# Kernel tuning notes

Measured on AMD Instinct MI355X. Metric: run time of the kernel, lower is better.

## Reference

```python
import jax, jax.numpy as jnp
import numpy as np
import math

B, L, DM, DI, DS, DR, K, NL = 1, 1024, 768, 1536, 16, 48, 4, 2
DT_MIN, DT_MAX = 0.001, 0.1


def rmsnorm(x, w, eps=1e-5):
    return x * jax.lax.rsqrt(jnp.mean(x * x, axis=-1, keepdims=True) + eps) * w


def causal_dwconv(x, w, b):
    # x: [B,L,C], w: [C,1,K]. torch Conv1d(padding=K-1)[..., :L] == left-pad K-1 causal conv.
    y = jax.lax.conv_general_dilated(
        x.transpose(0, 2, 1), w, (1,), [(K - 1, 0)],
        dimension_numbers=('NCH', 'OIH', 'NCH'), feature_group_count=DI)
    return y.transpose(0, 2, 1) + b


def selective_scan(x, delta, A, Bm, Cm, D):
    # x, delta: [B,L,DI]; A: [DI,DS]; Bm, Cm: [B,L,DS]; D: [DI]
    dA = jnp.exp(delta[..., None] * A)               # [B,L,DI,DS]
    BX = (delta * x)[..., None] * Bm[:, :, None, :]  # [B,L,DI,DS]

    def comb(c1, c2):
        a1, b1 = c1
        a2, b2 = c2
        return (a1 * a2, a2 * b1 + b2)

    _, hs = jax.lax.associative_scan(comb, (dA, BX), axis=1)  # h_t = dA_t*h_{t-1} + BX_t
    return jnp.einsum('bldn,bln->bld', hs, Cm) + D * x


def ssm(x, xproj_w, dt_w, dt_b, A_log, D):
    dbc = jnp.einsum('bld,ed->ble', x, xproj_w)            # [B,L,DR+2*DS]
    dlt, Bm, Cm = jnp.split(dbc, [DR, DR + DS], axis=-1)
    delta = jax.nn.softplus(jnp.einsum('blr,dr->bld', dlt, dt_w) + dt_b)
    return selective_scan(x, delta, -jnp.exp(A_log), Bm, Cm, D)


def mamba_block(x, p):
    xz = jnp.einsum('bld,ed->ble', x, p['in_w'])           # [B,L,2*DI]
    xin, z = jnp.split(xz, 2, axis=-1)
    xf = jax.nn.silu(causal_dwconv(xin, p['cf_w'], p['cf_b']))
    xb = jax.nn.silu(causal_dwconv(xin[:, ::-1, :], p['cb_w'], p['cb_b']))
    yf = ssm(xf, p['xf_w'], p['dtf_w'], p['dtf_b'], p['Af'], p['Df'])
    yb = ssm(xb, p['xb_w'], p['dtb_w'], p['dtb_b'], p['Ab'], p['Db'])  # NOT flipped back (faithful)
    y = jnp.einsum('ble,de->bld', jnp.concatenate([yf, yb], axis=-1), p['pro_w']) + p['pro_b']
    # tokenizer: scores over L, softmax along L, mix values; dropout = identity (eval)
    att = jax.nn.softmax(jnp.einsum('bld,td->btl', y, p['wA']), axis=-1)  # [B,T=L,L]
    vv = jnp.einsum('bld,de->ble', y, p['wV'])
    y = jnp.einsum('btl,ble->bte', att, vv)
    return jnp.einsum('bld,od->blo', y * jax.nn.silu(z), p['out_w'])


def reference(x, norm_w, in_proj_w, conv_f_w, conv_f_b, conv_b_w, conv_b_b,
              xproj_f_w, xproj_b_w, dt_f_w, dt_f_b, dt_b_w, dt_b_b,
              A_log_f, D_f, A_log_b, D_b, out_w, token_wA, token_wV, pro_w, pro_b):
    for i in range(NL):
        p = dict(in_w=in_proj_w[i], cf_w=conv_f_w[i], cf_b=conv_f_b[i],
                 cb_w=conv_b_w[i], cb_b=conv_b_b[i], xf_w=xproj_f_w[i],
                 xb_w=xproj_b_w[i], dtf_w=dt_f_w[i], dtf_b=dt_f_b[i],
                 dtb_w=dt_b_w[i], dtb_b=dt_b_b[i], Af=A_log_f[i], Df=D_f[i],
                 Ab=A_log_b[i], Db=D_b[i], out_w=out_w[i], wA=token_wA[i],
                 wV=token_wV[i], pro_w=pro_w[i], pro_b=pro_b[i])
        x = x + mamba_block(rmsnorm(x, norm_w[i]), p)
    return x


def setup_inputs():
    key = jax.random.key(0)
    ks = jax.random.split(key, 16)
    rn = lambda k, sh, s=0.02: jax.random.normal(k, sh, jnp.float32) * s
    A_log = jnp.broadcast_to(jnp.log(jnp.arange(1, DS + 1, dtype=jnp.float32)), (NL, DI, DS))
    dt = jnp.exp(jax.random.uniform(ks[0], (NL, DI)) * (math.log(DT_MAX) - math.log(DT_MIN)) + math.log(DT_MIN))
    inv_dt = dt + jnp.log(-jnp.expm1(-dt))  # softplus^-1(dt)
    dt_std = DR ** -0.5
    kaiming = (2.0 / DI) ** 0.5
    return {
        'x': jax.random.normal(ks[1], (B, L, DM), jnp.float32),
        'norm_w': jnp.ones((NL, DM), jnp.float32),
        'in_proj_w': rn(ks[2], (NL, 2 * DI, DM)),
        'conv_f_w': rn(ks[3], (NL, DI, 1, K), 0.3),
        'conv_f_b': jnp.zeros((NL, DI), jnp.float32),
        'conv_b_w': rn(ks[4], (NL, DI, 1, K), 0.3),
        'conv_b_b': jnp.zeros((NL, DI), jnp.float32),
        'xproj_f_w': rn(ks[5], (NL, DR + 2 * DS, DI)),
        'xproj_b_w': rn(ks[6], (NL, DR + 2 * DS, DI)),
        'dt_f_w': jax.random.uniform(ks[7], (NL, DI, DR), jnp.float32, -dt_std, dt_std),
        'dt_f_b': inv_dt,
        'dt_b_w': jax.random.uniform(ks[8], (NL, DI, DR), jnp.float32, -dt_std, dt_std),
        'dt_b_b': inv_dt,
        'A_log_f': A_log,
        'D_f': jnp.ones((NL, DI), jnp.float32),
        'A_log_b': A_log,
        'D_b': jnp.ones((NL, DI), jnp.float32),
        'out_w': rn(ks[9], (NL, DM, DI)),
        'token_wA': rn(ks[10], (NL, L, DI), kaiming),
        'token_wV': rn(ks[11], (NL, DI, DI), kaiming),
        'pro_w': rn(ks[12], (NL, DI, 2 * DI)),
        'pro_b': jnp.zeros((NL, DI), jnp.float32),
    }
```

## Files before the change

### kernel.cpp

```cpp
#include <hip/hip_runtime.h>
#include <hip/hip_bf16.h>
#include <math.h>
#include <stdint.h>

#define LSEQ 1024
#define DMODEL 768
#define DINNER 1536
#define DSTATE 16
#define DRANK 48
#define KCONV 4
#define NLAYER 2
#define DBC 80
#define NQ 8
#define QL (LSEQ / NQ)
#define SCH 8
#define SCW 32
#define QCH (QL / SCH)

typedef unsigned short u16;
typedef __attribute__((ext_vector_type(8))) __bf16 bf16x8;
typedef __attribute__((ext_vector_type(4))) float f32x4;
typedef __attribute__((ext_vector_type(4))) unsigned short us4;

__device__ __forceinline__ u16 f2bf(float f) {
  union { float f; unsigned u; } v; v.f = f;
  unsigned r = v.u + 0x7fffu + ((v.u >> 16) & 1u);
  return (u16)(r >> 16);
}
__device__ __forceinline__ float bf2f(u16 u) {
  union { unsigned u; float f; } v; v.u = ((unsigned)u) << 16;
  return v.f;
}

__device__ __forceinline__ void gload16(const void* g, void* l) {
  auto gp = reinterpret_cast<const __attribute__((address_space(1))) uint32_t*>(
      reinterpret_cast<uintptr_t>(g));
  auto lp = reinterpret_cast<__attribute__((address_space(3))) uint32_t*>(
      reinterpret_cast<uintptr_t>(l));
  __builtin_amdgcn_global_load_lds(gp, lp, 16, 0, 0);
}

#define CV0 589824
#define CV1 (CV0 + 1179648)
#define CV2 (CV1 + 393216)
#define CV3 (CV2 + 294912)
__global__ __launch_bounds__(256) void cvt4_k(
    const float* __restrict__ i0, u16* __restrict__ o0,
    const float* __restrict__ i1, u16* __restrict__ o1,
    const float* __restrict__ i2, u16* __restrict__ o2,
    const float* __restrict__ i3, u16* __restrict__ o3) {
  int i = blockIdx.x * 256 + threadIdx.x;
  const float* in; u16* out; int off;
  if (i < CV0)      { in = i0; out = o0; off = i; }
  else if (i < CV1) { in = i1; out = o1; off = i - CV0; }
  else if (i < CV2) { in = i2; out = o2; off = i - CV1; }
  else              { in = i3; out = o3; off = i - CV2; }
  float4 v = ((const float4*)in)[off];
  us4 o; o[0] = f2bf(v.x); o[1] = f2bf(v.y); o[2] = f2bf(v.z); o[3] = f2bf(v.w);
  ((us4*)out)[off] = o;
}

__global__ __launch_bounds__(256) void transcvt_k(const float* __restrict__ in,
                                                  u16* __restrict__ out,
                                                  int R, int C) {
  __shared__ float t[32][33];
  int c0 = blockIdx.x * 32, r0 = blockIdx.y * 32;
  int tx = threadIdx.x & 31, ty = threadIdx.x >> 5;
  for (int i = ty; i < 32; i += 8) t[i][tx] = in[(size_t)(r0 + i) * C + c0 + tx];
  __syncthreads();
  for (int i = ty; i < 32; i += 8)
    out[(size_t)(c0 + i) * R + r0 + tx] = f2bf(t[tx][i]);
}

__global__ __launch_bounds__(256) void transpose16_k(const u16* __restrict__ in,
                                                     u16* __restrict__ out,
                                                     int R, int C) {
  __shared__ u16 t[32][34];
  int c0 = blockIdx.x * 32, r0 = blockIdx.y * 32;
  int tx = threadIdx.x & 31, ty = threadIdx.x >> 5;
  for (int i = ty; i < 32; i += 8) t[i][tx] = in[(size_t)(r0 + i) * C + c0 + tx];
  __syncthreads();
  for (int i = ty; i < 32; i += 8)
    out[(size_t)(c0 + i) * R + r0 + tx] = t[tx][i];
}

__global__ __launch_bounds__(256) void rmsnorm_k(const float* __restrict__ x,
                                                 const float* __restrict__ w,
                                                 u16* __restrict__ xn) {
  int row = blockIdx.x;
  int tid = threadIdx.x;
  const float* xr = x + (size_t)row * DMODEL;
  float ss = 0.f;
  for (int j = tid; j < DMODEL; j += 256) { float v = xr[j]; ss += v * v; }
  __shared__ float red[256];
  red[tid] = ss; __syncthreads();
  for (int s = 128; s > 0; s >>= 1) { if (tid < s) red[tid] += red[tid + s]; __syncthreads(); }
  float scale = rsqrtf(red[0] / (float)DMODEL + 1e-5f);
  u16* outr = xn + (size_t)row * DMODEL;
  for (int j = tid; j < DMODEL; j += 256) outr[j] = f2bf(xr[j] * scale * w[j]);
}

template<int EPI>
__global__ __launch_bounds__(256) void mgemm_k(
    const u16* __restrict__ A, int lda,
    const u16* __restrict__ B, int ldb,
    void* __restrict__ Cv, int ldc, int K,
    const float* __restrict__ bias,
    const float* __restrict__ resid, int ldr)
{
  __shared__ u16 As[2][64 * 64];
  __shared__ u16 Bs[2][64 * 64];
  const int tid = threadIdx.x;
  const int lane = tid & 63;
  const int w = tid >> 6;

  const int nbx = gridDim.x;
  int bid = blockIdx.y * nbx + blockIdx.x;
  const int nwg = nbx * gridDim.y;
  bid = (bid & 7) * (nwg >> 3) + (bid >> 3);
  const int bm = (bid / nbx) * 64;
  const int bn = (bid % nbx) * 64;

  const int srow = lane >> 3;
  const int scs = (lane & 7) ^ srow;
  const int gA = 2 * w;
  const u16* Asrc0 = A + (size_t)(bm + gA * 8 + srow) * lda + scs * 8;
  const u16* Asrc1 = Asrc0 + (size_t)8 * lda;
  const u16* Bsrc0 = B + (size_t)(bn + gA * 8 + srow) * ldb + scs * 8;
  const u16* Bsrc1 = Bsrc0 + (size_t)8 * ldb;
  const int d0 = gA * 512;
  const int d1 = d0 + 512;

  const int fr = lane & 15;
  const int fs = lane >> 4;
  const int wm = (w >> 1) * 32;
  const int wn = (w & 1) * 32;
  int aoff[2][2], boff[2][2];
#pragma unroll
  for (int i = 0; i < 2; i++)
#pragma unroll
    for (int h = 0; h < 2; h++) {
      const int g = h * 4 + fs;
      aoff[i][h] = (wm + i * 16 + fr) * 64 + (g ^ (fr & 7)) * 8;
      boff[i][h] = (wn + i * 16 + fr) * 64 + (g ^ (fr & 7)) * 8;
    }

  f32x4 acc[2][2];
#pragma unroll
  for (int i = 0; i < 2; i++)
#pragma unroll
    for (int j = 0; j < 2; j++) acc[i][j] = (f32x4){0.f, 0.f, 0.f, 0.f};

#define STAGE(buf, k0) do { \
    gload16(Asrc0 + (k0), &As[buf][d0]); \
    gload16(Asrc1 + (k0), &As[buf][d1]); \
    gload16(Bsrc0 + (k0), &Bs[buf][d0]); \
    gload16(Bsrc1 + (k0), &Bs[buf][d1]); \
  } while (0)

  const int nk = K >> 6;
  STAGE(0, 0);

  for (int t = 0; t < nk; t++) {
    const int buf = t & 1;
    __syncthreads();
    if (t + 1 < nk) STAGE(buf ^ 1, (t + 1) << 6);
    const u16* As_ = As[buf];
    const u16* Bs_ = Bs[buf];
#pragma unroll
    for (int h = 0; h < 2; h++) {
      bf16x8 a0 = *reinterpret_cast<const bf16x8*>(As_ + aoff[0][h]);
      bf16x8 a1 = *reinterpret_cast<const bf16x8*>(As_ + aoff[1][h]);
      bf16x8 b0 = *reinterpret_cast<const bf16x8*>(Bs_ + boff[0][h]);
      bf16x8 b1 = *reinterpret_cast<const bf16x8*>(Bs_ + boff[1][h]);
      acc[0][0] = __builtin_amdgcn_mfma_f32_16x16x32_bf16(a0, b0, acc[0][0], 0, 0, 0);
      acc[0][1] = __builtin_amdgcn_mfma_f32_16x16x32_bf16(a0, b1, acc[0][1], 0, 0, 0);
      acc[1][0] = __builtin_amdgcn_mfma_f32_16x16x32_bf16(a1, b0, acc[1][0], 0, 0, 0);
      acc[1][1] = __builtin_amdgcn_mfma_f32_16x16x32_bf16(a1, b1, acc[1][1], 0, 0, 0);
    }
  }
#undef STAGE

#pragma unroll
  for (int i = 0; i < 2; i++) {
#pragma unroll
    for (int j = 0; j < 2; j++) {
      const int col = bn + wn + j * 16 + fr;
      const int row0 = bm + wm + i * 16 + fs * 4;
      float bv = (EPI & 1) ? bias[col] : 0.f;
#pragma unroll
      for (int r = 0; r < 4; r++) {
        float v = acc[i][j][r] + bv;
        if (EPI & 4) v += resid[(size_t)(row0 + r) * ldr + col];
        if (EPI & 16) {
          float z = (EPI & 32)
              ? bf2f(((const u16*)resid)[(size_t)(row0 + r) * ldr + col])
              : resid[(size_t)(row0 + r) * ldr + col];
          v *= z / (1.f + __expf(-z));
        }
        if (EPI & 8) ((u16*)Cv)[(size_t)(row0 + r) * ldc + col] = f2bf(v);
        else         ((float*)Cv)[(size_t)(row0 + r) * ldc + col] = v;
      }
    }
  }
}

__global__ __launch_bounds__(256) void svgemm_k(
    const u16* __restrict__ wA, const u16* __restrict__ ypro,
    const u16* __restrict__ wVT,
    float* __restrict__ Smat, u16* __restrict__ vv)
{
  __shared__ u16 As[2][64 * 64];
  __shared__ u16 Bs[2][64 * 64];
  const int tid = threadIdx.x;
  const int lane = tid & 63;
  const int w = tid >> 6;

  int bid = blockIdx.x;
  bid = (bid & 7) * 80 + (bid >> 3);
  const bool is_s = bid < 256;
  const u16* A;
  const u16* B;
  int bm, bn;
  if (is_s) { A = wA;   B = ypro; bm = (bid >> 4) * 64;         bn = (bid & 15) * 64; }
  else      { A = ypro; B = wVT;  bm = ((bid - 256) / 24) * 64; bn = ((bid - 256) % 24) * 64; }

  const int srow = lane >> 3;
  const int scs = (lane & 7) ^ srow;
  const int gA = 2 * w;
  const u16* Asrc0 = A + (size_t)(bm + gA * 8 + srow) * DINNER + scs * 8;
  const u16* Asrc1 = Asrc0 + (size_t)8 * DINNER;
  const u16* Bsrc0 = B + (size_t)(bn + gA * 8 + srow) * DINNER + scs * 8;
  const u16* Bsrc1 = Bsrc0 + (size_t)8 * DINNER;
  const int d0 = gA * 512;
  const int d1 = d0 + 512;

  const int fr = lane & 15;
  const int fs = lane >> 4;
  const int wm = (w >> 1) * 32;
  const int wn = (w & 1) * 32;
  int aoff[2][2], boff[2][2];
#pragma unroll
  for (int i = 0; i < 2; i++)
#pragma unroll
    for (int h = 0; h < 2; h++) {
      const int g = h * 4 + fs;
      aoff[i][h] = (wm + i * 16 + fr) * 64 + (g ^ (fr & 7)) * 8;
      boff[i][h] = (wn + i * 16 + fr) * 64 + (g ^ (fr & 7)) * 8;
    }

  f32x4 acc[2][2];
#pragma unroll
  for (int i = 0; i < 2; i++)
#pragma unroll
    for (int j = 0; j < 2; j++) acc[i][j] = (f32x4){0.f, 0.f, 0.f, 0.f};

#define STAGE(buf, k0) do { \
    gload16(Asrc0 + (k0), &As[buf][d0]); \
    gload16(Asrc1 + (k0), &As[buf][d1]); \
    gload16(Bsrc0 + (k0), &Bs[buf][d0]); \
    gload16(Bsrc1 + (k0), &Bs[buf][d1]); \
  } while (0)

  STAGE(0, 0);
  for (int t = 0; t < DINNER / 64; t++) {
    const int buf = t & 1;
    __syncthreads();
    if (t + 1 < DINNER / 64) STAGE(buf ^ 1, (t + 1) << 6);
    const u16* As_ = As[buf];
    const u16* Bs_ = Bs[buf];
#pragma unroll
    for (int h = 0; h < 2; h++) {
      bf16x8 a0 = *reinterpret_cast<const bf16x8*>(As_ + aoff[0][h]);
      bf16x8 a1 = *reinterpret_cast<const bf16x8*>(As_ + aoff[1][h]);
      bf16x8 b0 = *reinterpret_cast<const bf16x8*>(Bs_ + boff[0][h]);
      bf16x8 b1 = *reinterpret_cast<const bf16x8*>(Bs_ + boff[1][h]);
      acc[0][0] = __builtin_amdgcn_mfma_f32_16x16x32_bf16(a0, b0, acc[0][0], 0, 0, 0);
      acc[0][1] = __builtin_amdgcn_mfma_f32_16x16x32_bf16(a0, b1, acc[0][1], 0, 0, 0);
      acc[1][0] = __builtin_amdgcn_mfma_f32_16x16x32_bf16(a1, b0, acc[1][0], 0, 0, 0);
      acc[1][1] = __builtin_amdgcn_mfma_f32_16x16x32_bf16(a1, b1, acc[1][1], 0, 0, 0);
    }
  }
#undef STAGE

#pragma unroll
  for (int i = 0; i < 2; i++) {
#pragma unroll
    for (int j = 0; j < 2; j++) {
      const int col = bn + wn + j * 16 + fr;
      const int row0 = bm + wm + i * 16 + fs * 4;
#pragma unroll
      for (int r = 0; r < 4; r++) {
        float v = acc[i][j][r];
        if (is_s) Smat[(size_t)(row0 + r) * LSEQ + col] = v;
        else      vv[(size_t)(row0 + r) * DINNER + col] = f2bf(v);
      }
    }
  }
}

#define TG_R 16
#define TG_KC 96
#define TG_KS 16

__global__ __launch_bounds__(256) void thin_gemm_k(
    const u16* __restrict__ Af_, const u16* __restrict__ Ab_,
    const float* __restrict__ Bf_, const float* __restrict__ Bb_,
    float* __restrict__ partial)
{
  __shared__ u16 As[TG_R][TG_KC];
  __shared__ float Bs[80][100];
  const u16* A = blockIdx.z ? Ab_ : Af_;
  const float* B = blockIdx.z ? Bb_ : Bf_;
  float* part = partial + (size_t)blockIdx.z * TG_KS * LSEQ * DBC;
  const int tid = threadIdx.x;
  const int m0 = blockIdx.x * TG_R;
  const int ks = blockIdx.y;
  const int k0 = ks * TG_KC;

  for (int i = tid; i < 384; i += 256) {
    int r = i / 24, q = i % 24;
    *(us4*)&As[r][q * 4] = *(const us4*)(A + (size_t)(m0 + r) * DINNER + k0 + q * 4);
  }
  for (int i = tid; i < 1920; i += 256) {
    int r = i / 24, q = i % 24;
    *(float4*)&Bs[r][q * 4] = *(const float4*)(B + (size_t)r * DINNER + k0 + q * 4);
  }
  __syncthreads();

  const int r = tid >> 4;
  const int c0 = (tid & 15) * 5;
  float acc[5] = {};
  for (int k = 0; k < TG_KC; k++) {
    float a = bf2f(As[r][k]);
#pragma unroll
    for (int j = 0; j < 5; j++) acc[j] += a * Bs[c0 + j][k];
  }
  float* out = part + ((size_t)ks * LSEQ + m0 + r) * DBC + c0;
#pragma unroll
  for (int j = 0; j < 5; j++) out[j] = acc[j];
}

__global__ __launch_bounds__(256) void reduce_dbc_k(const float* __restrict__ partial,
                                                    float* __restrict__ outf,
                                                    float* __restrict__ outb) {
  int i = blockIdx.x * 256 + threadIdx.x;
  const float* part = partial + (size_t)blockIdx.y * TG_KS * LSEQ * DBC;
  float s = 0.f;
#pragma unroll
  for (int ks = 0; ks < TG_KS; ks++) s += part[(size_t)ks * (LSEQ * DBC) + i];
  (blockIdx.y ? outb : outf)[i] = s;
}

#define BM 64
#define BN 64
#define BK 16

__global__ __launch_bounds__(256) void delta_gemm_k(
    const float* __restrict__ A0, const float* __restrict__ A1,
    const float* __restrict__ B0, const float* __restrict__ B1,
    const float* __restrict__ b0, const float* __restrict__ b1,
    u16* __restrict__ C0, u16* __restrict__ C1)
{
  __shared__ float Asf[BK][BM];
  __shared__ float Bsf[BK][BN + 4];
  const float* A = blockIdx.z ? A1 : A0;
  const float* B = blockIdx.z ? B1 : B0;
  const float* bias = blockIdx.z ? b1 : b0;
  u16* C = blockIdx.z ? C1 : C0;
  const int tid = threadIdx.x;
  const int bm = blockIdx.y * BM;
  const int bn = blockIdx.x * BN;
  const int ar = tid >> 2;
  const int ak = (tid & 3) << 2;
  const int ty = tid >> 4, tx = tid & 15;
  float acc[4][4] = {};

  for (int k0 = 0; k0 < DRANK; k0 += BK) {
    float4 av = *(const float4*)(A + (size_t)(bm + ar) * DBC + k0 + ak);
    float4 bv = *(const float4*)(B + (size_t)(bn + ar) * DRANK + k0 + ak);
    __syncthreads();
    Asf[ak + 0][ar] = av.x; Asf[ak + 1][ar] = av.y;
    Asf[ak + 2][ar] = av.z; Asf[ak + 3][ar] = av.w;
    Bsf[ak + 0][ar] = bv.x; Bsf[ak + 1][ar] = bv.y;
    Bsf[ak + 2][ar] = bv.z; Bsf[ak + 3][ar] = bv.w;
    __syncthreads();
#pragma unroll
    for (int kk = 0; kk < BK; kk++) {
      float4 a4 = *(const float4*)&Asf[kk][ty * 4];
      float4 b4 = *(const float4*)&Bsf[kk][tx * 4];
      float a[4] = {a4.x, a4.y, a4.z, a4.w};
      float b[4] = {b4.x, b4.y, b4.z, b4.w};
#pragma unroll
      for (int i = 0; i < 4; i++)
#pragma unroll
        for (int j = 0; j < 4; j++)
          acc[i][j] += a[i] * b[j];
    }
  }

#pragma unroll
  for (int i = 0; i < 4; i++) {
    int row = bm + ty * 4 + i;
#pragma unroll
    for (int j = 0; j < 4; j++) {
      int col = bn + tx * 4 + j;
      float v = acc[i][j] + bias[col];
      v = (v > 20.f) ? v : log1pf(__expf(v));
      C[(size_t)row * DINNER + col] = f2bf(v);
    }
  }
}

__global__ __launch_bounds__(256) void conv_silu_k(
    const u16* __restrict__ xz,
    const float* __restrict__ wf, const float* __restrict__ bf,
    const float* __restrict__ wb, const float* __restrict__ bb,
    u16* __restrict__ xf, u16* __restrict__ xb)
{
  int idx = blockIdx.x * 256 + threadIdx.x;
  int dir = blockIdx.y;
  if (idx >= LSEQ * DINNER) return;
  int l = idx / DINNER, c = idx % DINNER;
  const float* w = (dir ? wb : wf) + c * KCONV;
  float acc = (dir ? bb : bf)[c];
#pragma unroll
  for (int k = 0; k < KCONV; k++) {
    int ls = l - (KCONV - 1) + k;
    if (ls >= 0) {
      int lsrc = dir ? (LSEQ - 1 - ls) : ls;
      acc += w[k] * bf2f(xz[(size_t)lsrc * (2 * DINNER) + c]);
    }
  }
  float sv = acc / (1.f + __expf(-acc));
  (dir ? xb : xf)[idx] = f2bf(sv);
}

__global__ __launch_bounds__(256) void scan_a_k(
    const u16* __restrict__ xcf, const u16* __restrict__ xcb,
    const u16* __restrict__ dltf, const u16* __restrict__ dltb,
    const float* __restrict__ dbcf, const float* __restrict__ dbcb,
    const float* __restrict__ Af, const float* __restrict__ Ab,
    float* __restrict__ qsP, float* __restrict__ qsQ)
{
  __shared__ float sP[SCH * SCW * DSTATE];
  __shared__ float sQ[SCH * SCW * DSTATE];
  const int dir = blockIdx.z;
  const int qid = blockIdx.y;
  const u16*   xc    = dir ? xcb : xcf;
  const u16*   delta = dir ? dltb : dltf;
  const float* dbc   = dir ? dbcb : dbcf;
  const float* A_log = dir ? Ab : Af;

  const int tid = threadIdx.x;
  const int c = tid >> 5;
  const int dl = tid & 31;
  const int d = blockIdx.x * SCW + dl;

  float Aa[DSTATE];
#pragma unroll
  for (int s = 0; s < DSTATE; s++) Aa[s] = -__expf(A_log[(size_t)d * DSTATE + s]);

  float aP[DSTATE], q[DSTATE];
#pragma unroll
  for (int s = 0; s < DSTATE; s++) { aP[s] = 1.f; q[s] = 0.f; }
  const int l0 = qid * QL + c * QCH;
  for (int i = 0; i < QCH; i++) {
    int l = l0 + i;
    float dt = bf2f(delta[(size_t)l * DINNER + d]);
    float dx = dt * bf2f(xc[(size_t)l * DINNER + d]);
    const float* bm = dbc + (size_t)l * DBC + DRANK;
#pragma unroll
    for (int s = 0; s < DSTATE; s++) {
      float a = __expf(dt * Aa[s]);
      q[s] = a * q[s] + dx * bm[s];
      aP[s] *= a;
    }
  }
#pragma unroll
  for (int s = 0; s < DSTATE; s++) {
    sP[(c * SCW + dl) * DSTATE + s] = aP[s];
    sQ[(c * SCW + dl) * DSTATE + s] = q[s];
  }
  __syncthreads();

#pragma unroll
  for (int pp = 0; pp < 2; pp++) {
    const int p = tid + pp * 256;
    const int d2 = p >> 4, s2 = p & 15;
    float h = 0.f, P = 1.f;
    for (int cc = 0; cc < SCH; cc++) {
      int idx = (cc * SCW + d2) * DSTATE + s2;
      h = sP[idx] * h + sQ[idx];
      P *= sP[idx];
    }
    size_t o = (((size_t)dir * NQ + qid) * DINNER + blockIdx.x * SCW + d2) * DSTATE + s2;
    qsP[o] = P;
    qsQ[o] = h;
  }
}

__global__ __launch_bounds__(256) void scan_c_k(
    const u16* __restrict__ xcf, const u16* __restrict__ xcb,
    const u16* __restrict__ dltf, const u16* __restrict__ dltb,
    const float* __restrict__ dbcf, const float* __restrict__ dbcb,
    const float* __restrict__ Af, const float* __restrict__ Ab,
    const float* __restrict__ Df, const float* __restrict__ Db,
    const float* __restrict__ qsP, const float* __restrict__ qsQ,
    u16* __restrict__ ycat)
{
  __shared__ float sP[SCH * SCW * DSTATE];
  __shared__ float sQ[SCH * SCW * DSTATE];
  const int dir = blockIdx.z;
  const int qid = blockIdx.y;
  const u16*   xc    = dir ? xcb : xcf;
  const u16*   delta = dir ? dltb : dltf;
  const float* dbc   = dir ? dbcb : dbcf;
  const float* A_log = dir ? Ab : Af;
  const float* Dvec  = dir ? Db : Df;
  const int col_off  = dir ? DINNER : 0;

  const int tid = threadIdx.x;
  const int c = tid >> 5;
  const int dl = tid & 31;
  const int d = blockIdx.x * SCW + dl;

  float Aa[DSTATE];
#pragma unroll
  for (int s = 0; s < DSTATE; s++) Aa[s] = -__expf(A_log[(size_t)d * DSTATE + s]);

  float aP[DSTATE], q[DSTATE];
#pragma unroll
  for (int s = 0; s < DSTATE; s++) { aP[s] = 1.f; q[s] = 0.f; }
  const int l0 = qid * QL + c * QCH;
  for (int i = 0; i < QCH; i++) {
    int l = l0 + i;
    float dt = bf2f(delta[(size_t)l * DINNER + d]);
    float dx = dt * bf2f(xc[(size_t)l * DINNER + d]);
    const float* bm = dbc + (size_t)l * DBC + DRANK;
#pragma unroll
    for (int s = 0; s < DSTATE; s++) {
      float a = __expf(dt * Aa[s]);
      q[s] = a * q[s] + dx * bm[s];
      aP[s] *= a;
    }
  }
#pragma unroll
  for (int s = 0; s < DSTATE; s++) {
    sP[(c * SCW + dl) * DSTATE + s] = aP[s];
    sQ[(c * SCW + dl) * DSTATE + s] = q[s];
  }
  __syncthreads();

#pragma unroll
  for (int pp = 0; pp < 2; pp++) {
    const int p = tid + pp * 256;
    const int d2 = p >> 4, s2 = p & 15;
    float h = 0.f;
    for (int qq = 0; qq < qid; qq++) {
      size_t o = (((size_t)dir * NQ + qq) * DINNER + blockIdx.x * SCW + d2) * DSTATE + s2;
      h = qsP[o] * h + qsQ[o];
    }
    for (int cc = 0; cc < SCH; cc++) {
      int idx = (cc * SCW + d2) * DSTATE + s2;
      float a = sP[idx], qv = sQ[idx];
      sP[idx] = h;
      h = a * h + qv;
    }
  }
  __syncthreads();

  float hs[DSTATE];
#pragma unroll
  for (int s = 0; s < DSTATE; s++) hs[s] = sP[(c * SCW + dl) * DSTATE + s];
  const float Dd = Dvec[d];
  for (int i = 0; i < QCH; i++) {
    int l = l0 + i;
    float dt = bf2f(delta[(size_t)l * DINNER + d]);
    float xv = bf2f(xc[(size_t)l * DINNER + d]);
    float dx = dt * xv;
    const float* bm = dbc + (size_t)l * DBC + DRANK;
    const float* cm = bm + DSTATE;
    float y = 0.f;
#pragma unroll
    for (int s = 0; s < DSTATE; s++) {
      float a = __expf(dt * Aa[s]);
      hs[s] = a * hs[s] + dx * bm[s];
      y += hs[s] * cm[s];
    }
    ycat[(size_t)l * (2 * DINNER) + col_off + d] = f2bf(y + Dd * xv);
  }
}

__global__ __launch_bounds__(256) void softmax_k(const float* __restrict__ S,
                                                 u16* __restrict__ P) {
  int row = blockIdx.x, tid = threadIdx.x;
  __shared__ float buf[LSEQ];
  __shared__ float red[256];
  const float* r = S + (size_t)row * LSEQ;
  float m = -1e30f;
  for (int j = tid; j < LSEQ; j += 256) { float v = r[j]; buf[j] = v; m = fmaxf(m, v); }
  red[tid] = m; __syncthreads();
  for (int s = 128; s > 0; s >>= 1) { if (tid < s) red[tid] = fmaxf(red[tid], red[tid + s]); __syncthreads(); }
  m = red[0];
  __syncthreads();
  float sum = 0.f;
  for (int j = tid; j < LSEQ; j += 256) { float e = __expf(buf[j] - m); buf[j] = e; sum += e; }
  red[tid] = sum; __syncthreads();
  for (int s = 128; s > 0; s >>= 1) { if (tid < s) red[tid] += red[tid + s]; __syncthreads(); }
  float inv = 1.f / red[0];
  u16* pr = P + (size_t)row * LSEQ;
  for (int j = tid; j < LSEQ; j += 256) pr[j] = f2bf(buf[j] * inv);
}

extern "C" void kernel_launch(void* const* d_in, const int* in_sizes, int n_in,
                              void* d_out, int out_size, void* d_ws, size_t ws_size,
                              hipStream_t stream) {
  const float* in_x      = (const float*)d_in[0];
  const float* norm_w    = (const float*)d_in[1];
  const float* in_proj_w = (const float*)d_in[2];
  const float* conv_f_w  = (const float*)d_in[3];
  const float* conv_f_b  = (const float*)d_in[4];
  const float* conv_b_w  = (const float*)d_in[5];
  const float* conv_b_b  = (const float*)d_in[6];
  const float* xproj_f_w = (const float*)d_in[7];
  const float* xproj_b_w = (const float*)d_in[8];
  const float* dt_f_w    = (const float*)d_in[9];
  const float* dt_f_b    = (const float*)d_in[10];
  const float* dt_b_w    = (const float*)d_in[11];
  const float* dt_b_b    = (const float*)d_in[12];
  const float* A_log_f   = (const float*)d_in[13];
  const float* D_f       = (const float*)d_in[14];
  const float* A_log_b   = (const float*)d_in[15];
  const float* D_b       = (const float*)d_in[16];
  const float* out_w     = (const float*)d_in[17];
  const float* token_wA  = (const float*)d_in[18];
  const float* token_wV  = (const float*)d_in[19];
  const float* pro_w     = (const float*)d_in[20];
  const float* pro_b     = (const float*)d_in[21];

  float* ws = (float*)d_ws;
  float* xbuf = ws; ws += LSEQ * DMODEL;
  u16* xz_bf  = (u16*)ws; ws += LSEQ * DINNER;
  u16* xf_bf  = (u16*)ws; ws += (LSEQ * DINNER) / 2;
  u16* xb_bf  = (u16*)ws; ws += (LSEQ * DINNER) / 2;
  float* dbcf = ws; ws += LSEQ * DBC;
  float* dbcb = ws; ws += LSEQ * DBC;
  float* delf_r = ws; ws += LSEQ * DINNER;
  float* delb_r = ws; ws += LSEQ * DINNER;
  float* scr  = ws; ws += LSEQ * DINNER;
  u16* xn_bf   = (u16*)ws; ws += (LSEQ * DMODEL) / 2;
  u16* ycat_bf = (u16*)ws; ws += LSEQ * DINNER;
  u16* ypro_bf = (u16*)ws; ws += (LSEQ * DINNER) / 2;
  u16* Wb      = (u16*)ws;
  u16* in_w_bf = Wb;
  u16* pw_bf   = in_w_bf + 3072 * 768;
  u16* wA_bf   = pw_bf + 1536 * 3072;
  u16* wVT_bf  = wA_bf + 1024 * 1536;
  u16* ow_bf   = wVT_bf + 1536 * 1536;

  float* dbc_part = delf_r;
  u16*   delf_bf  = (u16*)delf_r;
  u16*   delb_bf  = (u16*)delb_r;
  float* Smat     = delf_r;
  u16*   Smat_bf  = (u16*)delb_r;
  u16*   vv_bf    = xf_bf;
  u16*   vvT_bf   = xb_bf;
  u16*   g_bf     = ypro_bf;
  const int QS = 2 * NQ * DINNER * DSTATE;
  float* qsP   = scr;
  float* qsQ   = scr + QS;

  dim3 blk(256);
  for (int layer = 0; layer < NLAYER; layer++) {
    const float* nw  = norm_w    + (size_t)layer * DMODEL;
    const float* iw  = in_proj_w + (size_t)layer * 2 * DINNER * DMODEL;
    const float* cfw = conv_f_w  + (size_t)layer * DINNER * KCONV;
    const float* cfb = conv_f_b  + (size_t)layer * DINNER;
    const float* cbw = conv_b_w  + (size_t)layer * DINNER * KCONV;
    const float* cbb = conv_b_b  + (size_t)layer * DINNER;
    const float* xfw = xproj_f_w + (size_t)layer * DBC * DINNER;
    const float* xbw = xproj_b_w + (size_t)layer * DBC * DINNER;
    const float* dfw = dt_f_w    + (size_t)layer * DINNER * DRANK;
    const float* dfb = dt_f_b    + (size_t)layer * DINNER;
    const float* dbw = dt_b_w    + (size_t)layer * DINNER * DRANK;
    const float* dbb = dt_b_b    + (size_t)layer * DINNER;
    const float* Af  = A_log_f   + (size_t)layer * DINNER * DSTATE;
    const float* Df  = D_f       + (size_t)layer * DINNER;
    const float* Ab  = A_log_b   + (size_t)layer * DINNER * DSTATE;
    const float* Db  = D_b       + (size_t)layer * DINNER;
    const float* ow  = out_w     + (size_t)layer * DMODEL * DINNER;
    const float* wA  = token_wA  + (size_t)layer * LSEQ * DINNER;
    const float* wV  = token_wV  + (size_t)layer * DINNER * DINNER;
    const float* pw  = pro_w     + (size_t)layer * DINNER * 2 * DINNER;
    const float* pb  = pro_b     + (size_t)layer * DINNER;

    const float* xsrc = (layer == 0) ? in_x : xbuf;

    cvt4_k<<<CV3 / 256, blk, 0, stream>>>(iw, in_w_bf, pw, pw_bf, wA, wA_bf, ow, ow_bf);
    transcvt_k<<<dim3(1536 / 32, 1536 / 32), blk, 0, stream>>>(wV, wVT_bf, 1536, 1536);

    rmsnorm_k<<<LSEQ, blk, 0, stream>>>(xsrc, nw, xn_bf);

    mgemm_k<8><<<dim3(3072 / 64, LSEQ / 64), blk, 0, stream>>>(
        xn_bf, DMODEL, in_w_bf, DMODEL, xz_bf, 2 * DINNER, DMODEL, nullptr, nullptr, 0);

    conv_silu_k<<<dim3((LSEQ * DINNER) / 256, 2), blk, 0, stream>>>(
        xz_bf, cfw, cfb, cbw, cbb, xf_bf, xb_bf);

    thin_gemm_k<<<dim3(LSEQ / TG_R, TG_KS, 2), blk, 0, stream>>>(
        xf_bf, xb_bf, xfw, xbw, dbc_part);
    reduce_dbc_k<<<dim3((LSEQ * DBC) / 256, 2), blk, 0, stream>>>(
        dbc_part, dbcf, dbcb);

    delta_gemm_k<<<dim3(DINNER / BN, LSEQ / BM, 2), blk, 0, stream>>>(
        dbcf, dbcb, dfw, dbw, dfb, dbb, delf_bf, delb_bf);

    scan_a_k<<<dim3(DINNER / SCW, NQ, 2), blk, 0, stream>>>(
        xf_bf, xb_bf, delf_bf, delb_bf, dbcf, dbcb, Af, Ab, qsP, qsQ);
    scan_c_k<<<dim3(DINNER / SCW, NQ, 2), blk, 0, stream>>>(
        xf_bf, xb_bf, delf_bf, delb_bf, dbcf, dbcb, Af, Ab, Df, Db, qsP, qsQ, ycat_bf);

    mgemm_k<9><<<dim3(DINNER / 64, LSEQ / 64), blk, 0, stream>>>(
        ycat_bf, 2 * DINNER, pw_bf, 2 * DINNER, ypro_bf, DINNER, 2 * DINNER,
        pb, nullptr, 0);

    svgemm_k<<<640, blk, 0, stream>>>(wA_bf, ypro_bf, wVT_bf, Smat, vv_bf);
    softmax_k<<<LSEQ, blk, 0, stream>>>(Smat, Smat_bf);

    transpose16_k<<<dim3(DINNER / 32, LSEQ / 32), blk, 0, stream>>>(
        vv_bf, vvT_bf, LSEQ, DINNER);

    mgemm_k<56><<<dim3(DINNER / 64, LSEQ / 64), blk, 0, stream>>>(
        Smat_bf, LSEQ, vvT_bf, LSEQ, g_bf, DINNER, LSEQ,
        nullptr, (const float*)(xz_bf + DINNER), 2 * DINNER);

    float* target = (layer == NLAYER - 1) ? (float*)d_out : xbuf;
    mgemm_k<4><<<dim3(DMODEL / 64, LSEQ / 64), blk, 0, stream>>>(
        g_bf, DINNER, ow_bf, DINNER, target, DMODEL, DINNER,
        nullptr, xsrc, DMODEL);
  }
}
```

Measured before the change: 413.8 us.

## Batch weight conversion, widen GEMM tiles, fuse vv transpose into svgemm epilogue

Converts both layers' weights to bf16 in single launches before the layer loop, storing per-layer copies. Adds a 64x128-tile MFMA GEMM used for the in-proj, pro-proj and attention-mix GEMMs to increase operand reuse per block. The svgemm kernel now writes vv already transposed through a small LDS tile, which removes the separate transpose kernel. scan_a launches one fewer chunk row. These cut launches and memory traffic but need more workspace for two layers of bf16 weights and use a larger LDS footprint per block.

New measurement: 416.0 us. No clear change (+0.5%).

```diff
diff --git a/kernel.cpp b/kernel.cpp
--- a/kernel.cpp
+++ b/kernel.cpp
@@ -44,44 +44,36 @@
 #define CV1 (CV0 + 1179648)
 #define CV2 (CV1 + 393216)
 #define CV3 (CV2 + 294912)
+#define WBL 12189696
 __global__ __launch_bounds__(256) void cvt4_k(
-    const float* __restrict__ i0, u16* __restrict__ o0,
-    const float* __restrict__ i1, u16* __restrict__ o1,
-    const float* __restrict__ i2, u16* __restrict__ o2,
-    const float* __restrict__ i3, u16* __restrict__ o3) {
+    const float* __restrict__ i0, u16* __restrict__ o0, int s0o,
+    const float* __restrict__ i1, u16* __restrict__ o1, int s1o,
+    const float* __restrict__ i2, u16* __restrict__ o2, int s2o,
+    const float* __restrict__ i3, u16* __restrict__ o3, int s3o) {
   int i = blockIdx.x * 256 + threadIdx.x;
+  int lay = blockIdx.y;
   const float* in; u16* out; int off;
-  if (i < CV0)      { in = i0; out = o0; off = i; }
-  else if (i < CV1) { in = i1; out = o1; off = i - CV0; }
-  else if (i < CV2) { in = i2; out = o2; off = i - CV1; }
-  else              { in = i3; out = o3; off = i - CV2; }
+  if (i < CV0)      { in = i0 + (size_t)lay * s0o * 4; out = o0 + (size_t)lay * WBL; off = i; }
+  else if (i < CV1) { in = i1 + (size_t)lay * s1o * 4; out = o1 + (size_t)lay * WBL; off = i - CV0; }
+  else if (i < CV2) { in = i2 + (size_t)lay * s2o * 4; out = o2 + (size_t)lay * WBL; off = i - CV1; }
+  else              { in = i3 + (size_t)lay * s3o * 4; out = o3 + (size_t)lay * WBL; off = i - CV2; }
   float4 v = ((const float4*)in)[off];
   us4 o; o[0] = f2bf(v.x); o[1] = f2bf(v.y); o[2] = f2bf(v.z); o[3] = f2bf(v.w);
   ((us4*)out)[off] = o;
 }
 
-__global__ __launch_bounds__(256) void transcvt_k(const float* __restrict__ in,
-                                                  u16* __restrict__ out,
+__global__ __launch_bounds__(256) void transcvt_k(const float* __restrict__ in0,
+                                                  u16* __restrict__ out0,
                                                   int R, int C) {
   __shared__ float t[32][33];
+  const float* in = in0 + (size_t)blockIdx.z * R * C;
+  u16* out = out0 + (size_t)blockIdx.z * WBL;
   int c0 = blockIdx.x * 32, r0 = blockIdx.y * 32;
   int tx = threadIdx.x & 31, ty = threadIdx.x >> 5;
   for (int i = ty; i < 32; i += 8) t[i][tx] = in[(size_t)(r0 + i) * C + c0 + tx];
   __syncthreads();
   for (int i = ty; i < 32; i += 8)
     out[(size_t)(c0 + i) * R + r0 + tx] = f2bf(t[tx][i]);
-}
-
-__global__ __launch_bounds__(256) void transpose16_k(const u16* __restrict__ in,
-                                                     u16* __restrict__ out,
-                                                     int R, int C) {
-  __shared__ u16 t[32][34];
-  int c0 = blockIdx.x * 32, r0 = blockIdx.y * 32;
-  int tx = threadIdx.x & 31, ty = threadIdx.x >> 5;
-  for (int i = ty; i < 32; i += 8) t[i][tx] = in[(size_t)(r0 + i) * C + c0 + tx];
-  __syncthreads();
-  for (int i = ty; i < 32; i += 8)
-    out[(size_t)(c0 + i) * R + r0 + tx] = t[tx][i];
 }
 
 __global__ __launch_bounds__(256) void rmsnorm_k(const float* __restrict__ x,
@@ -205,13 +197,123 @@
   }
 }
 
+template<int EPI>
+__global__ __launch_bounds__(256) void mgemmW_k(
+    const u16* __restrict__ A, int lda,
+    const u16* __restrict__ B, int ldb,
+    void* __restrict__ Cv, int ldc, int K,
+    const float* __restrict__ bias,
+    const float* __restrict__ resid, int ldr)
+{
+  __shared__ u16 As[2][64 * 64];
+  __shared__ u16 Bs[2][128 * 64];
+  const int tid = threadIdx.x;
+  const int lane = tid & 63;
+  const int w = tid >> 6;
+
+  const int nbx = gridDim.x;
+  int bid = blockIdx.y * nbx + blockIdx.x;
+  const int nwg = nbx * gridDim.y;
+  bid = (bid & 7) * (nwg >> 3) + (bid >> 3);
+  const int bm = (bid / nbx) * 64;
+  const int bn = (bid % nbx) * 128;
+
+  const int srow = lane >> 3;
+  const int scs = (lane & 7) ^ srow;
+  const u16* Asrc0 = A + (size_t)(bm + (2 * w) * 8 + srow) * lda + scs * 8;
+  const u16* Asrc1 = Asrc0 + (size_t)8 * lda;
+  const int da0 = (2 * w) * 512, da1 = da0 + 512;
+  const u16* Bsrc0 = B + (size_t)(bn + (4 * w) * 8 + srow) * ldb + scs * 8;
+  const u16* Bsrc1 = Bsrc0 + (size_t)8 * ldb;
+  const u16* Bsrc2 = Bsrc1 + (size_t)8 * ldb;
+  const u16* Bsrc3 = Bsrc2 + (size_t)8 * ldb;
+  const int db0 = (4 * w) * 512;
+
+  const int fr = lane & 15;
+  const int fs = lane >> 4;
+  const int wm = (w >> 1) * 32;
+  const int wn = (w & 1) * 64;
+  int aoff[2][2], boff[4][2];
+#pragma unroll
+  for (int h = 0; h < 2; h++) {
+    const int g = h * 4 + fs;
+    const int sw = (g ^ (fr & 7)) * 8;
+#pragma unroll
+    for (int i = 0; i < 2; i++) aoff[i][h] = (wm + i * 16 + fr) * 64 + sw;
+#pragma unroll
+    for (int j = 0; j < 4; j++) boff[j][h] = (wn + j * 16 + fr) * 64 + sw;
+  }
+
+  f32x4 acc[2][4];
+#pragma unroll
+  for (int i = 0; i < 2; i++)
+#pragma unroll
+    for (int j = 0; j < 4; j++) acc[i][j] = (f32x4){0.f, 0.f, 0.f, 0.f};
+
+#define STAGEW(buf, k0) do { \
+    gload16(Asrc0 + (k0), &As[buf][da0]); \
+    gload16(Asrc1 + (k0), &As[buf][da1]); \
+    gload16(Bsrc0 + (k0), &Bs[buf][db0]); \
+    gload16(Bsrc1 + (k0), &Bs[buf][db0 + 512]); \
+    gload16(Bsrc2 + (k0), &Bs[buf][db0 + 1024]); \
+    gload16(Bsrc3 + (k0), &Bs[buf][db0 + 1536]); \
+  } while (0)
+
+  const int nk = K >> 6;
+  STAGEW(0, 0);
+
+  for (int t = 0; t < nk; t++) {
+    const int buf = t & 1;
+    __syncthreads();
+    if (t + 1 < nk) STAGEW(buf ^ 1, (t + 1) << 6);
+    const u16* As_ = As[buf];
+    const u16* Bs_ = Bs[buf];
+#pragma unroll
+    for (int h = 0; h < 2; h++) {
+      bf16x8 a0 = *reinterpret_cast<const bf16x8*>(As_ + aoff[0][h]);
+      bf16x8 a1 = *reinterpret_cast<const bf16x8*>(As_ + aoff[1][h]);
+#pragma unroll
+      for (int j = 0; j < 4; j++) {
+        bf16x8 b = *reinterpret_cast<const bf16x8*>(Bs_ + boff[j][h]);
+        acc[0][j] = __builtin_amdgcn_mfma_f32_16x16x32_bf16(a0, b, acc[0][j], 0, 0, 0);
+        acc[1][j] = __builtin_amdgcn_mfma_f32_16x16x32_bf16(a1, b, acc[1][j], 0, 0, 0);
+      }
+    }
+  }
+#undef STAGEW
+
+#pragma unroll
+  for (int i = 0; i < 2; i++) {
+#pragma unroll
+    for (int j = 0; j < 4; j++) {
+      const int col = bn + wn + j * 16 + fr;
+      const int row0 = bm + wm + i * 16 + fs * 4;
+      float bv = (EPI & 1) ? bias[col] : 0.f;
+#pragma unroll
+      for (int r = 0; r < 4; r++) {
+        float v = acc[i][j][r] + bv;
+        if (EPI & 4) v += resid[(size_t)(row0 + r) * ldr + col];
+        if (EPI & 16) {
+          float z = (EPI & 32)
+              ? bf2f(((const u16*)resid)[(size_t)(row0 + r) * ldr + col])
+              : resid[(size_t)(row0 + r) * ldr + col];
+          v *= z / (1.f + __expf(-z));
+        }
+        if (EPI & 8) ((u16*)Cv)[(size_t)(row0 + r) * ldc + col] = f2bf(v);
+        else         ((float*)Cv)[(size_t)(row0 + r) * ldc + col] = v;
+      }
+    }
+  }
+}
+
 __global__ __launch_bounds__(256) void svgemm_k(
     const u16* __restrict__ wA, const u16* __restrict__ ypro,
     const u16* __restrict__ wVT,
-    float* __restrict__ Smat, u16* __restrict__ vv)
+    float* __restrict__ Smat, u16* __restrict__ vvT)
 {
   __shared__ u16 As[2][64 * 64];
   __shared__ u16 Bs[2][64 * 64];
+  __shared__ u16 tr[4][32][33];
   const int tid = threadIdx.x;
   const int lane = tid & 63;
   const int w = tid >> 6;
@@ -283,18 +385,39 @@
   }
 #undef STAGE
 
-#pragma unroll
-  for (int i = 0; i < 2; i++) {
-#pragma unroll
-    for (int j = 0; j < 2; j++) {
-      const int col = bn + wn + j * 16 + fr;
-      const int row0 = bm + wm + i * 16 + fs * 4;
-#pragma unroll
-      for (int r = 0; r < 4; r++) {
-        float v = acc[i][j][r];
-        if (is_s) Smat[(size_t)(row0 + r) * LSEQ + col] = v;
-        else      vv[(size_t)(row0 + r) * DINNER + col] = f2bf(v);
+  if (is_s) {
+#pragma unroll
+    for (int i = 0; i < 2; i++)
+#pragma unroll
+      for (int j = 0; j < 2; j++) {
+        const int col = bn + wn + j * 16 + fr;
+        const int row0 = bm + wm + i * 16 + fs * 4;
+#pragma unroll
+        for (int r = 0; r < 4; r++)
+          Smat[(size_t)(row0 + r) * LSEQ + col] = acc[i][j][r];
       }
+  } else {
+#pragma unroll
+    for (int i = 0; i < 2; i++)
+#pragma unroll
+      for (int j = 0; j < 2; j++) {
+        const int lr0 = i * 16 + fs * 4;
+        const int lc = j * 16 + fr;
+#pragma unroll
+        for (int r = 0; r < 4; r++) tr[w][lr0 + r][lc] = f2bf(acc[i][j][r]);
+      }
+    __syncthreads();
+    const int lc = lane >> 1;
+    const int half = lane & 1;
+    const int gcol = bn + wn + lc;
+    const int grow0 = bm + wm + half * 16;
+    u16* dst = vvT + (size_t)gcol * LSEQ + grow0;
+#pragma unroll
+    for (int q = 0; q < 4; q++) {
+      us4 v;
+#pragma unroll
+      for (int e = 0; e < 4; e++) v[e] = tr[w][half * 16 + q * 4 + e][lc];
+      *(us4*)(dst + q * 4) = v;
     }
   }
 }
@@ -653,18 +776,18 @@
   u16* ycat_bf = (u16*)ws; ws += LSEQ * DINNER;
   u16* ypro_bf = (u16*)ws; ws += (LSEQ * DINNER) / 2;
   u16* Wb      = (u16*)ws;
-  u16* in_w_bf = Wb;
-  u16* pw_bf   = in_w_bf + 3072 * 768;
-  u16* wA_bf   = pw_bf + 1536 * 3072;
-  u16* wVT_bf  = wA_bf + 1024 * 1536;
-  u16* ow_bf   = wVT_bf + 1536 * 1536;
+
+  u16* in_w_bf0 = Wb;
+  u16* pw_bf0   = in_w_bf0 + 3072 * 768;
+  u16* wA_bf0   = pw_bf0 + 1536 * 3072;
+  u16* wVT_bf0  = wA_bf0 + 1024 * 1536;
+  u16* ow_bf0   = wVT_bf0 + 1536 * 1536;
 
   float* dbc_part = delf_r;
   u16*   delf_bf  = (u16*)delf_r;
   u16*   delb_bf  = (u16*)delb_r;
   float* Smat     = delf_r;
   u16*   Smat_bf  = (u16*)delb_r;
-  u16*   vv_bf    = xf_bf;
   u16*   vvT_bf   = xb_bf;
   u16*   g_bf     = ypro_bf;
   const int QS = 2 * NQ * DINNER * DSTATE;
@@ -672,9 +795,17 @@
   float* qsQ   = scr + QS;
 
   dim3 blk(256);
+
+  cvt4_k<<<dim3(CV3 / 256, NLAYER), blk, 0, stream>>>(
+      in_proj_w, in_w_bf0, 2 * DINNER * DMODEL / 4,
+      pro_w,     pw_bf0,   DINNER * 2 * DINNER / 4,
+      token_wA,  wA_bf0,   LSEQ * DINNER / 4,
+      out_w,     ow_bf0,   DMODEL * DINNER / 4);
+  transcvt_k<<<dim3(1536 / 32, 1536 / 32, NLAYER), blk, 0, stream>>>(
+      token_wV, wVT_bf0, 1536, 1536);
+
   for (int layer = 0; layer < NLAYER; layer++) {
     const float* nw  = norm_w    + (size_t)layer * DMODEL;
-    const float* iw  = in_proj_w + (size_t)layer * 2 * DINNER * DMODEL;
     const float* cfw = conv_f_w  + (size_t)layer * DINNER * KCONV;
     const float* cfb = conv_f_b  + (size_t)layer * DINNER;
     const float* cbw = conv_b_w  + (size_t)layer * DINNER * KCONV;
@@ -689,20 +820,19 @@
     const float* Df  = D_f       + (size_t)layer * DINNER;
     const float* Ab  = A_log_b   + (size_t)layer * DINNER * DSTATE;
     const float* Db  = D_b       + (size_t)layer * DINNER;
-    const float* ow  = out_w     + (size_t)layer * DMODEL * DINNER;
-    const float* wA  = token_wA  + (size_t)layer * LSEQ * DINNER;
-    const float* wV  = token_wV  + (size_t)layer * DINNER * DINNER;
-    const float* pw  = pro_w     + (size_t)layer * DINNER * 2 * DINNER;
     const float* pb  = pro_b     + (size_t)layer * DINNER;
 
+    u16* in_w_bf = in_w_bf0 + (size_t)layer * WBL;
+    u16* pw_bf   = pw_bf0   + (size_t)layer * WBL;
+    u16* wA_bf   = wA_bf0   + (size_t)layer * WBL;
+    u16* wVT_bf  = wVT_bf0  + (size_t)layer * WBL;
+    u16* ow_bf   = ow_bf0   + (size_t)layer * WBL;
+
     const float* xsrc = (layer == 0) ? in_x : xbuf;
 
-    cvt4_k<<<CV3 / 256, blk, 0, stream>>>(iw, in_w_bf, pw, pw_bf, wA, wA_bf, ow, ow_bf);
-    transcvt_k<<<dim3(1536 / 32, 1536 / 32), blk, 0, stream>>>(wV, wVT_bf, 1536, 1536);
-
     rmsnorm_k<<<LSEQ, blk, 0, stream>>>(xsrc, nw, xn_bf);
 
-    mgemm_k<8><<<dim3(3072 / 64, LSEQ / 64), blk, 0, stream>>>(
+    mgemmW_k<8><<<dim3(3072 / 128, LSEQ / 64), blk, 0, stream>>>(
         xn_bf, DMODEL, in_w_bf, DMODEL, xz_bf, 2 * DINNER, DMODEL, nullptr, nullptr, 0);
 
     conv_silu_k<<<dim3((LSEQ * DINNER) / 256, 2), blk, 0, stream>>>(
@@ -716,22 +846,19 @@
     delta_gemm_k<<<dim3(DINNER / BN, LSEQ / BM, 2), blk, 0, stream>>>(
         dbcf, dbcb, dfw, dbw, dfb, dbb, delf_bf, delb_bf);
 
-    scan_a_k<<<dim3(DINNER / SCW, NQ, 2), blk, 0, stream>>>(
+    scan_a_k<<<dim3(DINNER / SCW, NQ - 1, 2), blk, 0, stream>>>(
         xf_bf, xb_bf, delf_bf, delb_bf, dbcf, dbcb, Af, Ab, qsP, qsQ);
     scan_c_k<<<dim3(DINNER / SCW, NQ, 2), blk, 0, stream>>>(
         xf_bf, xb_bf, delf_bf, delb_bf, dbcf, dbcb, Af, Ab, Df, Db, qsP, qsQ, ycat_bf);
 
-    mgemm_k<9><<<dim3(DINNER / 64, LSEQ / 64), blk, 0, stream>>>(
+    mgemmW_k<9><<<dim3(DINNER / 128, LSEQ / 64), blk, 0, stream>>>(
         ycat_bf, 2 * DINNER, pw_bf, 2 * DINNER, ypro_bf, DINNER, 2 * DINNER,
         pb, nullptr, 0);
 
-    svgemm_k<<<640, blk, 0, stream>>>(wA_bf, ypro_bf, wVT_bf, Smat, vv_bf);
+    svgemm_k<<<640, blk, 0, stream>>>(wA_bf, ypro_bf, wVT_bf, Smat, vvT_bf);
     softmax_k<<<LSEQ, blk, 0, stream>>>(Smat, Smat_bf);
 
-    transpose16_k<<<dim3(DINNER / 32, LSEQ / 32), blk, 0, stream>>>(
-        vv_bf, vvT_bf, LSEQ, DINNER);
-
-    mgemm_k<56><<<dim3(DINNER / 64, LSEQ / 64), blk, 0, stream>>>(
+    mgemmW_k<56><<<dim3(DINNER / 128, LSEQ / 64), blk, 0, stream>>>(
         Smat_bf, LSEQ, vvT_bf, LSEQ, g_bf, DINNER, LSEQ,
         nullptr, (const float*)(xz_bf + DINNER), 2 * DINNER);
 
```
